# Kernel tuning notes

Measured on AMD Instinct MI355X. Metric: run time of the kernel, lower is better.

The kernel has to match this reference:

```python
import jax, jax.numpy as jnp
import numpy as np

HEAD = 8
D_Q = 64
NEG_INF = -1e9
EPS = 1e-9


def setup_inputs() -> dict:
    key = jax.random.key(0)
    ks = jax.random.split(key, 5)
    bs, seq_len, d_model = 4, 1024, 512
    context = jax.random.normal(ks[0], (bs, seq_len, d_model), dtype=jnp.float32)
    attention_mask = jnp.ones((bs, seq_len), dtype=jnp.int32)
    # nn.Linear default init: U(-1/sqrt(fan_in), 1/sqrt(fan_in))
    bound = 1.0 / np.sqrt(d_model)
    Wq = jax.random.uniform(ks[1], (HEAD * D_Q, d_model), jnp.float32, -bound, bound)
    bq = jax.random.uniform(ks[2], (HEAD * D_Q,), jnp.float32, -bound, bound)
    Wk = jax.random.uniform(ks[3], (HEAD * D_Q, d_model), jnp.float32, -bound, bound)
    bk = jax.random.uniform(ks[4], (HEAD * D_Q,), jnp.float32, -bound, bound)
    return {"context": context, "attention_mask": attention_mask,
            "Wq": Wq, "bq": bq, "Wk": Wk, "bk": bk}


def reference(context, attention_mask, Wq, bq, Wk, bk):
    bs, seq_len, d_model = context.shape
    # structural masks
    after_mask = jnp.eye(seq_len, k=1, dtype=jnp.int32)    # superdiagonal
    prev_mask = jnp.eye(seq_len, k=-1, dtype=jnp.int32)    # subdiagonal
    self_mask = jnp.eye(seq_len, dtype=jnp.int32)          # diagonal
    summing_op = jnp.triu(jnp.ones((seq_len, seq_len), jnp.float32))  # upper-tri ones

    # attention_mask & (after + prev): (bs,1,1,S) & (S,S) -> (bs,1,S,S)
    mask = attention_mask[:, None, None, :] & (after_mask + prev_mask)

    # projections -> (bs, head, seq, d_q)
    q = (context @ Wq.T + bq).reshape(bs, seq_len, HEAD, D_Q).transpose(0, 2, 1, 3)
    k = (context @ Wk.T + bk).reshape(bs, seq_len, HEAD, D_Q).transpose(0, 2, 1, 3)

    scores = jnp.einsum('bhqd,bhkd->bhqk', q, k) / d_model
    scores = jnp.where(mask == 0, NEG_INF, scores)
    scores = jax.nn.softmax(scores, axis=-1)

    # geometric-mean fusion of forward/backward neighbor scores
    phrasal_attn = jnp.sqrt(scores * jnp.swapaxes(scores, -2, -1) + EPS)
    # prior_attn = 0 (default): phrasal_attn = 0 + (1-0)*phrasal_attn

    # log-cumsum via triangular matmuls
    p = jnp.where(after_mask == 0, 0.0, jnp.log(phrasal_attn + EPS))  # (bs,h,S,S)
    p = jnp.einsum('bhij,jk->bhik', p, summing_op)
    attn = jnp.exp(jnp.einsum('ij,bhjk->bhik', summing_op, p))
    # zero out on-and-below diagonal (keep strict upper triangle)
    strict_upper = summing_op.astype(jnp.int32) - self_mask
    attn = jnp.where(strict_upper == 0, 0.0, attn)
    attn = attn + jnp.swapaxes(attn, -2, -1) + jnp.where(self_mask == 0, EPS, phrasal_attn)
    return (attn, phrasal_attn)
```

## Files before the change

### kernel.cpp

```cpp
#include <hip/hip_runtime.h>
#include <hip/hip_bf16.h>

#define BS 4
#define SEQ 1024
#define DM 512
#define NQK 1024
#define NROW (BS*SEQ)
#define EPS 1e-9f
#define SQRTEPS 3.16227766e-5f

typedef __attribute__((ext_vector_type(8))) short short8;
typedef __attribute__((ext_vector_type(4))) float floatx4;

__global__ __launch_bounds__(256) void convert_kernel(
    const float* __restrict__ ctx, const float* __restrict__ Wq,
    const float* __restrict__ Wk, unsigned short* __restrict__ Xbf,
    unsigned short* __restrict__ Wbf)
{
    int idx = blockIdx.x * 256 + threadIdx.x;
    {
        unsigned int u = __float_as_uint(ctx[idx]);
        Xbf[idx] = (unsigned short)((u + 0x7fffu + ((u >> 16) & 1u)) >> 16);
    }
    if (idx < DM * DM) {
        unsigned int a = __float_as_uint(Wq[idx]);
        Wbf[idx] = (unsigned short)((a + 0x7fffu + ((a >> 16) & 1u)) >> 16);
        unsigned int c = __float_as_uint(Wk[idx]);
        Wbf[DM * DM + idx] = (unsigned short)((c + 0x7fffu + ((c >> 16) & 1u)) >> 16);
    }
}

#define BM 128
#define BN 128
#define BK 32
#define LDA 40

__global__ __launch_bounds__(256) void gemm_qk(
    const unsigned short* __restrict__ X, const unsigned short* __restrict__ W,
    const float* __restrict__ bq, const float* __restrict__ bk,
    float* __restrict__ QK)
{
    __shared__ unsigned short As[BM * LDA];
    __shared__ unsigned short Bs[BN * LDA];

    const int tid  = threadIdx.x;
    const int bm   = blockIdx.x;
    const int bn   = blockIdx.y;
    const int wave = tid >> 6;
    const int lane = tid & 63;
    const int wm   = wave >> 1, wn = wave & 1;
    const int lr   = lane & 15;
    const int kg   = lane >> 4;

    floatx4 acc[4][4] = {};

    for (int k0 = 0; k0 < DM; k0 += BK) {
        __syncthreads();
        #pragma unroll
        for (int p = 0; p < 2; ++p) {
            int c   = tid + p * 256;
            int row = c >> 2;
            int kc  = (c & 3) << 3;
            uint4 va = *(const uint4*)(X + (size_t)(bm * BM + row) * DM + k0 + kc);
            *(uint4*)(As + row * LDA + kc) = va;
            uint4 vb = *(const uint4*)(W + (size_t)(bn * BN + row) * DM + k0 + kc);
            *(uint4*)(Bs + row * LDA + kc) = vb;
        }
        __syncthreads();

        short8 a[4], b[4];
        #pragma unroll
        for (int mi = 0; mi < 4; ++mi)
            a[mi] = *(const short8*)(As + (wm * 64 + mi * 16 + lr) * LDA + kg * 8);
        #pragma unroll
        for (int ni = 0; ni < 4; ++ni)
            b[ni] = *(const short8*)(Bs + (wn * 64 + ni * 16 + lr) * LDA + kg * 8);
        #pragma unroll
        for (int mi = 0; mi < 4; ++mi)
            #pragma unroll
            for (int ni = 0; ni < 4; ++ni)
                acc[mi][ni] = __builtin_amdgcn_mfma_f32_16x16x32_bf16(
                    a[mi], b[ni], acc[mi][ni], 0, 0, 0);
    }

    #pragma unroll
    for (int mi = 0; mi < 4; ++mi) {
        #pragma unroll
        for (int ni = 0; ni < 4; ++ni) {
            int n = bn * BN + wn * 64 + ni * 16 + lr;
            float bias = (n < DM) ? bq[n] : bk[n - DM];
            #pragma unroll
            for (int r = 0; r < 4; ++r) {
                int m = bm * BM + wm * 64 + mi * 16 + kg * 4 + r;
                QK[(size_t)m * NQK + n] = acc[mi][ni][r] + bias;
            }
        }
    }
}

__global__ __launch_bounds__(1024) void scan_kernel(
    const float* __restrict__ QK, const int* __restrict__ am,
    float* __restrict__ gArr, float* __restrict__ CArr)
{
    __shared__ float uS[SEQ], vS[SEQ];
    __shared__ double sc[SEQ];

    const int bh = blockIdx.x;
    const int b  = bh >> 3, h = bh & 7;
    const int i  = threadIdx.x;

    float u = 0.f, v = 0.f;
    if (i < SEQ - 1) {
        const floatx4* qi  = (const floatx4*)(QK + (size_t)(b * SEQ + i)     * NQK + h * 64);
        const floatx4* ki1 = (const floatx4*)(QK + (size_t)(b * SEQ + i + 1) * NQK + DM + h * 64);
        const floatx4* qi1 = (const floatx4*)(QK + (size_t)(b * SEQ + i + 1) * NQK + h * 64);
        const floatx4* ki  = (const floatx4*)(QK + (size_t)(b * SEQ + i)     * NQK + DM + h * 64);
        float su = 0.f, sv = 0.f;
        #pragma unroll
        for (int t = 0; t < 16; ++t) {
            floatx4 a = qi[t], c = ki1[t], d = qi1[t], e = ki[t];
            su += a.x * c.x + a.y * c.y + a.z * c.z + a.w * c.w;
            sv += d.x * e.x + d.y * e.y + d.z * e.z + d.w * e.w;
        }
        u = su * (1.0f / DM);
        v = sv * (1.0f / DM);
    }
    uS[i] = u; vS[i] = v;
    __syncthreads();

    float g = 0.f;
    if (i < SEQ - 1) {
        int mL = (i > 0) ? am[b * SEQ + i - 1] : 0;
        int mR = am[b * SEQ + i + 1];
        float s_up = mR ? (mL ? 1.f / (1.f + expf(vS[i - 1] - u)) : 1.f) : 0.f;
        int mL2 = am[b * SEQ + i];
        int mR2 = (i + 2 < SEQ) ? am[b * SEQ + i + 2] : 0;
        float s_dn = mL2 ? (mR2 ? 1.f / (1.f + expf(uS[i + 1] - v)) : 1.f) : 0.f;
        g = sqrtf(s_up * s_dn + EPS);
        gArr[bh * SEQ + i] = g;
    }

    double x = (i < SEQ - 1) ? (double)logf(g + EPS) : 0.0;
    sc[i] = x;
    __syncthreads();
    #pragma unroll
    for (int off = 1; off < SEQ; off <<= 1) {
        double t = (i >= off) ? sc[i - off] : 0.0;
        __syncthreads();
        sc[i] += t;
        __syncthreads();
    }
    CArr[bh * SEQ + i] = (i == 0) ? 0.f : (float)sc[i - 1];
}

__global__ __launch_bounds__(256) void fill_kernel(
    const float* __restrict__ gArr, const float* __restrict__ CArr,
    float* __restrict__ attn, float* __restrict__ phrasal)
{
    const int row = blockIdx.x;
    const int bh  = row >> 10;
    const int i   = row & 1023;
    const int t   = threadIdx.x;

    const float Ci  = CArr[row];
    const float gm1 = (i > 0)       ? gArr[bh * SEQ + i - 1] : 0.f;
    const float gp  = (i < SEQ - 1) ? gArr[bh * SEQ + i]     : 0.f;

    floatx4 c4 = *(const floatx4*)(CArr + bh * SEQ + t * 4);
    floatx4 av, pv;
    #pragma unroll
    for (int j = 0; j < 4; ++j) {
        int k = t * 4 + j;
        float ck = c4[j];
        float d  = (k > i) ? (ck - Ci) : (Ci - ck);
        av[j] = (k == i) ? SQRTEPS : (__expf(d) + EPS);
        pv[j] = (k == i - 1) ? gm1 : ((k == i + 1) ? gp : SQRTEPS);
    }
    *(floatx4*)(attn    + (size_t)row * SEQ + t * 4) = av;
    *(floatx4*)(phrasal + (size_t)row * SEQ + t * 4) = pv;
}

extern "C" void kernel_launch(void* const* d_in, const int* in_sizes, int n_in,
                              void* d_out, int out_size, void* d_ws, size_t ws_size,
                              hipStream_t stream) {
    const float* ctx = (const float*)d_in[0];
    const int*   am  = (const int*)d_in[1];
    const float* Wq  = (const float*)d_in[2];
    const float* bq  = (const float*)d_in[3];
    const float* Wk  = (const float*)d_in[4];
    const float* bk  = (const float*)d_in[5];
    float* out = (float*)d_out;

    char* ws = (char*)d_ws;
    unsigned short* Xbf = (unsigned short*)(ws);
    unsigned short* Wbf = (unsigned short*)(ws + 4194304);
    float*          QK  = (float*)(ws + 5242880);
    float*          gA  = (float*)(ws + 22020096);
    float*          CA  = (float*)(ws + 22151168);

    convert_kernel<<<dim3(BS * SEQ * DM / 256), 256, 0, stream>>>(ctx, Wq, Wk, Xbf, Wbf);
    gemm_qk<<<dim3(NROW / BM, NQK / BN), 256, 0, stream>>>(Xbf, Wbf, bq, bk, QK);
    scan_kernel<<<dim3(BS * 8), 1024, 0, stream>>>(QK, am, gA, CA);

    float* attn_out    = out;
    float* phrasal_out = out + (size_t)BS * 8 * SEQ * SEQ;
    fill_kernel<<<dim3(BS * 8 * SEQ), 256, 0, stream>>>(gA, CA, attn_out, phrasal_out);
}
```

Measured before the change: 332.3 us.

## Shrink GEMM tiles and split dot/scan into wave-parallel kernels

The projection GEMM tile drops from 128x128 to 64x64 so the grid has more blocks, and each global load is issued before the barrier to overlap it a little. The old 32-block scan kernel, which computed neighbour dot products serially per thread and ran a shared-memory scan with many barriers, is split in two. A new kernel computes each dot product with one wave and shuffle reductions across many blocks, and the scan now uses wave shuffles plus a small per-wave prefix table. This adds an extra launch and a small intermediate buffer, and the smaller GEMM tiles reuse less data per block.

```diff
diff --git a/kernel.cpp b/kernel.cpp
--- a/kernel.cpp
+++ b/kernel.cpp
@@ -30,8 +30,8 @@
     }
 }
 
-#define BM 128
-#define BN 128
+#define BM 64
+#define BN 64
 #define BK 32
 #define LDA 40
 
@@ -52,105 +52,121 @@
     const int lr   = lane & 15;
     const int kg   = lane >> 4;
 
-    floatx4 acc[4][4] = {};
+    const int srow = tid >> 2;
+    const int skc  = (tid & 3) << 3;
+    const unsigned short* Xp = X + (size_t)(bm * BM + srow) * DM + skc;
+    const unsigned short* Wp = W + (size_t)(bn * BN + srow) * DM + skc;
+
+    floatx4 acc[2][2] = {};
 
     for (int k0 = 0; k0 < DM; k0 += BK) {
+        uint4 va = *(const uint4*)(Xp + k0);
+        uint4 vb = *(const uint4*)(Wp + k0);
         __syncthreads();
-        #pragma unroll
-        for (int p = 0; p < 2; ++p) {
-            int c   = tid + p * 256;
-            int row = c >> 2;
-            int kc  = (c & 3) << 3;
-            uint4 va = *(const uint4*)(X + (size_t)(bm * BM + row) * DM + k0 + kc);
-            *(uint4*)(As + row * LDA + kc) = va;
-            uint4 vb = *(const uint4*)(W + (size_t)(bn * BN + row) * DM + k0 + kc);
-            *(uint4*)(Bs + row * LDA + kc) = vb;
-        }
+        *(uint4*)(As + srow * LDA + skc) = va;
+        *(uint4*)(Bs + srow * LDA + skc) = vb;
         __syncthreads();
 
-        short8 a[4], b[4];
-        #pragma unroll
-        for (int mi = 0; mi < 4; ++mi)
-            a[mi] = *(const short8*)(As + (wm * 64 + mi * 16 + lr) * LDA + kg * 8);
-        #pragma unroll
-        for (int ni = 0; ni < 4; ++ni)
-            b[ni] = *(const short8*)(Bs + (wn * 64 + ni * 16 + lr) * LDA + kg * 8);
-        #pragma unroll
-        for (int mi = 0; mi < 4; ++mi)
+        short8 a[2], b[2];
+        #pragma unroll
+        for (int mi = 0; mi < 2; ++mi)
+            a[mi] = *(const short8*)(As + (wm * 32 + mi * 16 + lr) * LDA + kg * 8);
+        #pragma unroll
+        for (int ni = 0; ni < 2; ++ni)
+            b[ni] = *(const short8*)(Bs + (wn * 32 + ni * 16 + lr) * LDA + kg * 8);
+        #pragma unroll
+        for (int mi = 0; mi < 2; ++mi)
             #pragma unroll
-            for (int ni = 0; ni < 4; ++ni)
+            for (int ni = 0; ni < 2; ++ni)
                 acc[mi][ni] = __builtin_amdgcn_mfma_f32_16x16x32_bf16(
                     a[mi], b[ni], acc[mi][ni], 0, 0, 0);
     }
 
     #pragma unroll
-    for (int mi = 0; mi < 4; ++mi) {
-        #pragma unroll
-        for (int ni = 0; ni < 4; ++ni) {
-            int n = bn * BN + wn * 64 + ni * 16 + lr;
+    for (int mi = 0; mi < 2; ++mi) {
+        #pragma unroll
+        for (int ni = 0; ni < 2; ++ni) {
+            int n = bn * BN + wn * 32 + ni * 16 + lr;
             float bias = (n < DM) ? bq[n] : bk[n - DM];
             #pragma unroll
             for (int r = 0; r < 4; ++r) {
-                int m = bm * BM + wm * 64 + mi * 16 + kg * 4 + r;
+                int m = bm * BM + wm * 32 + mi * 16 + kg * 4 + r;
                 QK[(size_t)m * NQK + n] = acc[mi][ni][r] + bias;
             }
         }
     }
 }
 
-__global__ __launch_bounds__(1024) void scan_kernel(
-    const float* __restrict__ QK, const int* __restrict__ am,
-    float* __restrict__ gArr, float* __restrict__ CArr)
-{
-    __shared__ float uS[SEQ], vS[SEQ];
-    __shared__ double sc[SEQ];
-
-    const int bh = blockIdx.x;
-    const int b  = bh >> 3, h = bh & 7;
-    const int i  = threadIdx.x;
+__global__ __launch_bounds__(256) void dot_kernel(
+    const float* __restrict__ QK, float* __restrict__ uArr, float* __restrict__ vArr)
+{
+    const int gw   = blockIdx.x * 4 + (threadIdx.x >> 6);
+    const int lane = threadIdx.x & 63;
+    const int bh   = gw >> 10;
+    const int i    = gw & 1023;
+    const int b    = bh >> 3, h = bh & 7;
 
     float u = 0.f, v = 0.f;
     if (i < SEQ - 1) {
-        const floatx4* qi  = (const floatx4*)(QK + (size_t)(b * SEQ + i)     * NQK + h * 64);
-        const floatx4* ki1 = (const floatx4*)(QK + (size_t)(b * SEQ + i + 1) * NQK + DM + h * 64);
-        const floatx4* qi1 = (const floatx4*)(QK + (size_t)(b * SEQ + i + 1) * NQK + h * 64);
-        const floatx4* ki  = (const floatx4*)(QK + (size_t)(b * SEQ + i)     * NQK + DM + h * 64);
-        float su = 0.f, sv = 0.f;
-        #pragma unroll
-        for (int t = 0; t < 16; ++t) {
-            floatx4 a = qi[t], c = ki1[t], d = qi1[t], e = ki[t];
-            su += a.x * c.x + a.y * c.y + a.z * c.z + a.w * c.w;
-            sv += d.x * e.x + d.y * e.y + d.z * e.z + d.w * e.w;
+        const float* r0 = QK + (size_t)(b * SEQ + i)     * NQK;
+        const float* r1 = QK + (size_t)(b * SEQ + i + 1) * NQK;
+        float qi  = r0[h * 64 + lane];
+        float ki  = r0[DM + h * 64 + lane];
+        float qi1 = r1[h * 64 + lane];
+        float ki1 = r1[DM + h * 64 + lane];
+        float pu = qi * ki1, pv = qi1 * ki;
+        #pragma unroll
+        for (int m = 1; m < 64; m <<= 1) {
+            pu += __shfl_xor(pu, m);
+            pv += __shfl_xor(pv, m);
         }
-        u = su * (1.0f / DM);
-        v = sv * (1.0f / DM);
-    }
-    uS[i] = u; vS[i] = v;
-    __syncthreads();
+        u = pu * (1.0f / DM);
+        v = pv * (1.0f / DM);
+    }
+    if (lane == 0) { uArr[gw] = u; vArr[gw] = v; }
+}
+
+__global__ __launch_bounds__(1024) void gscan_kernel(
+    const float* __restrict__ uArr, const float* __restrict__ vArr,
+    const int* __restrict__ am, float* __restrict__ gArr, float* __restrict__ CArr)
+{
+    __shared__ double wsum[16];
+
+    const int bh   = blockIdx.x;
+    const int b    = bh >> 3;
+    const int i    = threadIdx.x;
+    const int base = bh * SEQ;
 
     float g = 0.f;
     if (i < SEQ - 1) {
+        float u   = uArr[base + i];
+        float vv  = vArr[base + i];
+        int   im1 = (i > 0) ? i - 1 : 0;
+        float vm1 = vArr[base + im1];
+        float up1 = uArr[base + i + 1];
         int mL = (i > 0) ? am[b * SEQ + i - 1] : 0;
         int mR = am[b * SEQ + i + 1];
-        float s_up = mR ? (mL ? 1.f / (1.f + expf(vS[i - 1] - u)) : 1.f) : 0.f;
+        float s_up = mR ? (mL ? 1.f / (1.f + expf(vm1 - u)) : 1.f) : 0.f;
         int mL2 = am[b * SEQ + i];
         int mR2 = (i + 2 < SEQ) ? am[b * SEQ + i + 2] : 0;
-        float s_dn = mL2 ? (mR2 ? 1.f / (1.f + expf(uS[i + 1] - v)) : 1.f) : 0.f;
+        float s_dn = mL2 ? (mR2 ? 1.f / (1.f + expf(up1 - vv)) : 1.f) : 0.f;
         g = sqrtf(s_up * s_dn + EPS);
-        gArr[bh * SEQ + i] = g;
-    }
-
-    double x = (i < SEQ - 1) ? (double)logf(g + EPS) : 0.0;
-    sc[i] = x;
+        gArr[base + i] = g;
+    }
+
+    double L = (i < SEQ - 1) ? (double)logf(g + EPS) : 0.0;
+    double x = L;
+    const int lane = i & 63, wv = i >> 6;
+    #pragma unroll
+    for (int off = 1; off < 64; off <<= 1) {
+        double t = __shfl_up(x, off);
+        if (lane >= off) x += t;
+    }
+    if (lane == 63) wsum[wv] = x;
     __syncthreads();
-    #pragma unroll
-    for (int off = 1; off < SEQ; off <<= 1) {
-        double t = (i >= off) ? sc[i - off] : 0.0;
-        __syncthreads();
-        sc[i] += t;
-        __syncthreads();
-    }
-    CArr[bh * SEQ + i] = (i == 0) ? 0.f : (float)sc[i - 1];
+    double pref = 0.0;
+    for (int w = 0; w < wv; ++w) pref += wsum[w];
+    CArr[base + i] = (float)(pref + x - L);
 }
 
 __global__ __launch_bounds__(256) void fill_kernel(
@@ -195,12 +211,15 @@
     unsigned short* Xbf = (unsigned short*)(ws);
     unsigned short* Wbf = (unsigned short*)(ws + 4194304);
     float*          QK  = (float*)(ws + 5242880);
-    float*          gA  = (float*)(ws + 22020096);
-    float*          CA  = (float*)(ws + 22151168);
+    float*          uA  = (float*)(ws + 22020096);
+    float*          vA  = (float*)(ws + 22151168);
+    float*          gA  = (float*)(ws + 22282240);
+    float*          CA  = (float*)(ws + 22413312);
 
     convert_kernel<<<dim3(BS * SEQ * DM / 256), 256, 0, stream>>>(ctx, Wq, Wk, Xbf, Wbf);
     gemm_qk<<<dim3(NROW / BM, NQK / BN), 256, 0, stream>>>(Xbf, Wbf, bq, bk, QK);
-    scan_kernel<<<dim3(BS * 8), 1024, 0, stream>>>(QK, am, gA, CA);
+    dot_kernel<<<dim3(BS * 8 * SEQ / 4), 256, 0, stream>>>(QK, uA, vA);
+    gscan_kernel<<<dim3(BS * 8), 1024, 0, stream>>>(uA, vA, am, gA, CA);
 
     float* attn_out    = out;
     float* phrasal_out = out + (size_t)BS * 8 * SEQ * SEQ;
```

Result: faster. 300.9 us (-9.4%).
